# Kernel optimization log

Hardware: AMD Instinct MI355X
Metric: run time of the kernel (lower is better)

Reference implementation:

```python
import jax, jax.numpy as jnp
import numpy as np

N_SRC, N_DST = 1000, 1000
N = N_SRC + N_DST          # 2000 == feat_in of SW MLP (hard-coded in original)
D = 128                    # metapath2vec embedding dim
H = 256                    # SW hidden width
B = 100000                 # skip-gram (center, context) pairs
K = 5                      # negatives per pair
EP = 200000                # positive-graph edges
EN = 200000                # negative-graph edges


def setup_inputs() -> dict:
    key = jax.random.key(0)
    ks = jax.random.split(key, 12)
    node_embed = jax.random.normal(ks[0], (N, D), jnp.float32) * 0.1
    context_embed = jax.random.normal(ks[1], (N, D), jnp.float32) * 0.1
    # symmetric bipartite adjacency: etype plus its reverse asetype, homogenized
    A = (jax.random.uniform(ks[2], (N_SRC, N_DST)) < 0.02).astype(jnp.float32)
    adj = jnp.block([[jnp.zeros((N_SRC, N_SRC), jnp.float32), A],
                     [A.T, jnp.zeros((N_DST, N_DST), jnp.float32)]])
    W1 = jax.random.normal(ks[3], (N, H), jnp.float32) / np.sqrt(N).astype(np.float32)
    b1 = jnp.zeros((H,), jnp.float32)
    W2 = jax.random.normal(ks[4], (H, D), jnp.float32) / np.sqrt(H).astype(np.float32)
    b2 = jnp.zeros((D,), jnp.float32)
    pos_u = jax.random.randint(ks[5], (B,), 0, N)
    pos_v = jax.random.randint(ks[6], (B,), 0, N)
    neg_v = jax.random.randint(ks[7], (B, K), 0, N)
    pos_src = jax.random.randint(ks[8], (EP,), 0, N_SRC)
    pos_dst = jax.random.randint(ks[9], (EP,), 0, N_DST)
    neg_src = jax.random.randint(ks[10], (EN,), 0, N_SRC)
    neg_dst = jax.random.randint(ks[11], (EN,), 0, N_DST)
    return dict(node_embed=node_embed, context_embed=context_embed, adj=adj,
                W1=W1, b1=b1, W2=W2, b2=b2,
                pos_u=pos_u, pos_v=pos_v, neg_v=neg_v,
                pos_src=pos_src, pos_dst=pos_dst,
                neg_src=neg_src, neg_dst=neg_dst)


def _skipgram_loss(node_embed, context_embed, pos_u, pos_v, neg_v):
    # DGL MetaPath2Vec negative-sampling skip-gram loss
    emb_u = node_embed[pos_u]            # [B, D] gather
    emb_v = context_embed[pos_v]         # [B, D] gather
    pos = jnp.clip(jnp.sum(emb_u * emb_v, axis=-1), -10.0, 10.0)
    pos_loss = -jax.nn.log_sigmoid(pos)
    emb_neg = context_embed[neg_v]       # [B, K, D] gather
    neg = jnp.clip(jnp.einsum('bkd,bd->bk', emb_neg, emb_u), -10.0, 10.0)
    neg_loss = -jnp.sum(jax.nn.log_sigmoid(-neg), axis=-1)
    return jnp.mean(pos_loss + neg_loss)


def _sw_embedding(adj, feats, W1, b1, W2, b2):
    # adj @ adj @ adj * adj  /  outer(diag(adj@adj))  -> L2-row-normalized -> MLP
    A2 = adj @ adj                       # [N, N]
    part1 = (A2 @ adj) * adj             # 3-path counts masked onto existing edges
    d = jnp.diag(A2)                     # [N]
    part2 = d[:, None] * d[None, :]      # outer product of 2-path counts
    ok = part2 > 0
    gamma = jnp.where(ok, part1 / jnp.where(ok, part2, 1.0), 0.0)  # == nan_to_num
    norm = jnp.sqrt(jnp.sum(gamma * gamma, axis=-1, keepdims=True))
    gamma = gamma / jnp.maximum(norm, 1e-12)          # F.normalize(p=2, dim=1)
    sw_h = jnp.tanh(gamma @ W1 + b1) @ W2 + b2        # [N, 128]
    return jnp.concatenate([feats, sw_h], axis=1)     # [N, 256]


def reference(node_embed, context_embed, adj, W1, b1, W2, b2,
              pos_u, pos_v, neg_v, pos_src, pos_dst, neg_src, neg_dst):
    loss = _skipgram_loss(node_embed, context_embed, pos_u, pos_v, neg_v)
    # feats[etype[0]] ++ feats[etype[2]] == full node_embed table in global order
    h = _sw_embedding(adj, node_embed, W1, b1, W2, b2)
    h_src, h_dst = h[:N_SRC], h[N_SRC:]
    # HeteroDotPredictor: u_dot_v per edge -> [E, 1]
    pos_score = jnp.sum(h_src[pos_src] * h_dst[pos_dst], axis=-1, keepdims=True)
    neg_score = jnp.sum(h_src[neg_src] * h_dst[neg_dst], axis=-1, keepdims=True)
    return loss, pos_score, neg_score
```

## Files before the change

kernel.cpp:

```cpp
#include <hip/hip_runtime.h>
#include <hip/hip_bf16.h>

typedef __attribute__((ext_vector_type(8))) short bf16x8;
typedef __attribute__((ext_vector_type(4))) float f32x4;
typedef unsigned short u16;

#define BATCH 100000
#define EPE 200000

#define OFF_AP    ((size_t)0)
#define OFF_ATP   ((size_t)2097152)
#define OFF_SP    ((size_t)4194304)
#define OFF_T1    ((size_t)6291456)
#define OFF_G     ((size_t)6291456)
#define OFF_GT    ((size_t)10485760)
#define OFF_GNS   ((size_t)14680064)
#define OFF_GNDT  ((size_t)16777216)
#define OFF_W1AT  ((size_t)18874368)
#define OFF_W1BT  ((size_t)19398656)
#define OFF_W2T   ((size_t)19922944)
#define OFF_HID   ((size_t)19988480)
#define OFF_NEP   ((size_t)21037056)
#define OFF_CEP   ((size_t)21561344)
#define OFF_HSRC  ((size_t)22085632)
#define OFF_HDST  ((size_t)22609920)
#define OFF_T2    ((size_t)23134208)
#define OFF_DEGS  ((size_t)27328512)
#define OFF_DEGD  ((size_t)27332608)
#define OFF_PART  ((size_t)27336704)

__device__ __forceinline__ u16 f2b(float f) {
  union { float f; unsigned u; } v; v.f = f;
  unsigned r = v.u + 0x7fffu + ((v.u >> 16) & 1u);
  return (u16)(r >> 16);
}
__device__ __forceinline__ float b2f(u16 h) {
  union { unsigned u; float f; } v; v.u = ((unsigned)h) << 16;
  return v.f;
}

#define AS1C(p) ((const __attribute__((address_space(1))) void*)(p))
#define AS3(p)  ((__attribute__((address_space(3))) void*)(p))

__global__ __launch_bounds__(256) void prep(const float* __restrict__ adj,
    const float* __restrict__ W1, const float* __restrict__ W2,
    const float* __restrict__ ne, const float* __restrict__ ce,
    u16* __restrict__ Ap, u16* __restrict__ ATp,
    u16* __restrict__ W1At, u16* __restrict__ W1Bt, u16* __restrict__ w2t,
    u16* __restrict__ nep, u16* __restrict__ cep,
    u16* __restrict__ hsrcp, u16* __restrict__ hdstp,
    float* __restrict__ degd, float* __restrict__ degs) {
  __shared__ float tile[64][65];
  __shared__ float redf[256];
  int b = blockIdx.x;
  int t = threadIdx.x;
  int tx = t & 63, ty = t >> 6;
  if (b < 256) {
    int tr = b >> 4, tc = b & 15;
    #pragma unroll
    for (int p = 0; p < 16; p++) {
      int r = p * 4 + ty;
      int gr = tr * 64 + r, gc = tc * 64 + tx;
      float v = (gr < 1000 && gc < 1000) ? adj[(size_t)gr * 2000 + 1000 + gc] : 0.f;
      Ap[(size_t)gr * 1024 + gc] = f2b(v);
      tile[r][tx] = v;
    }
    __syncthreads();
    #pragma unroll
    for (int p = 0; p < 16; p++) {
      int r = p * 4 + ty;
      ATp[(size_t)(tc * 64 + r) * 1024 + tr * 64 + tx] = f2b(tile[tx][r]);
    }
  } else if (b < 384) {
    int b2 = b - 256;
    int half = b2 >> 6, rem = b2 & 63;
    int jt = rem >> 2, ht = rem & 3;
    #pragma unroll
    for (int p = 0; p < 16; p++) {
      int r = p * 4 + ty;
      int j = jt * 64 + r;
      tile[r][tx] = (j < 1000) ? W1[(size_t)(half * 1000 + j) * 256 + ht * 64 + tx] : 0.f;
    }
    __syncthreads();
    u16* outp = half ? W1Bt : W1At;
    #pragma unroll
    for (int p = 0; p < 16; p++) {
      int r = p * 4 + ty;
      outp[(size_t)(ht * 64 + r) * 1024 + jt * 64 + tx] = f2b(tile[tx][r]);
    }
  } else if (b < 392) {
    int b3 = b - 384;
    int dt = b3 >> 2, kt = b3 & 3;
    #pragma unroll
    for (int p = 0; p < 16; p++) {
      int r = p * 4 + ty;
      tile[r][tx] = W2[(size_t)(kt * 64 + r) * 128 + dt * 64 + tx];
    }
    __syncthreads();
    #pragma unroll
    for (int p = 0; p < 16; p++) {
      int r = p * 4 + ty;
      w2t[(size_t)(dt * 64 + r) * 256 + kt * 64 + tx] = f2b(tile[tx][r]);
    }
  } else if (b < 1416) {
    int idx = (b - 392) * 256 + t;
    int i = idx >> 7, d = idx & 127;
    float nv = (i < 2000) ? ne[(size_t)i * 128 + d] : 0.f;
    float cv = (i < 2000) ? ce[(size_t)i * 128 + d] : 0.f;
    u16 nb = f2b(nv);
    nep[idx] = nb;
    cep[idx] = f2b(cv);
    if (i < 1000)                   hsrcp[(size_t)i * 256 + d] = nb;
    else if (i < 1024)              hsrcp[(size_t)i * 256 + d] = 0;
    if (i >= 1000 && i < 2000)      hdstp[(size_t)(i - 1000) * 256 + d] = nb;
    else if (i >= 2000 && i < 2024) hdstp[(size_t)(i - 1000) * 256 + d] = 0;
  } else if (b < 1448) {
    int jb = b - 1416;
    int cx = t & 31, ry = t >> 5;
    int j = jb * 32 + cx;
    float s = 0.f;
    if (j < 1000)
      for (int i = ry; i < 1000; i += 8) s += adj[(size_t)i * 2000 + 1000 + j];
    redf[t] = s;
    __syncthreads();
    if (ry == 0) {
      float tot = 0.f;
      #pragma unroll
      for (int k = 0; k < 8; k++) tot += redf[k * 32 + cx];
      degd[j] = (j < 1000) ? tot : 0.f;
    }
  } else {
    int ib = b - 1448;
    int r = t >> 3, c8 = t & 7;
    int i = ib * 32 + r;
    float s = 0.f;
    if (i < 1000)
      for (int k = c8; k < 1000; k += 8) s += adj[(size_t)i * 2000 + 1000 + k];
    redf[t] = s;
    __syncthreads();
    if (c8 == 0) {
      float tot = 0.f;
      #pragma unroll
      for (int k = 0; k < 8; k++) tot += redf[r * 8 + k];
      degs[i] = (i < 1000) ? tot : 0.f;
    }
  }
}

template <int EPI, int MR, int NR>
__global__ __launch_bounds__(256) void gemm_bt(
    const u16* __restrict__ A, const u16* __restrict__ BT,
    const u16* __restrict__ A2, const u16* __restrict__ BT2,
    int K, int lda, int ldbt,
    u16* __restrict__ outb, int ldo,
    float* __restrict__ outf,
    const u16* __restrict__ apack,
    const float* __restrict__ degs, const float* __restrict__ degd,
    const float* __restrict__ bias,
    u16* __restrict__ hsrcp, u16* __restrict__ hdstp,
    float* __restrict__ outf2)
{
  constexpr int BMt = 32 * MR, BNt = 32 * NR;
  __shared__ u16 As[2][BMt * 64];
  __shared__ u16 Bs[2][BNt * 64];
  const int t = threadIdx.x;
  const int w = t >> 6, lane = t & 63;
  const int brow = blockIdx.x * BMt, bcol = blockIdx.y * BNt;
  const int wr = w >> 1, wc = w & 1;
  const int r16 = lane & 15, kg = lane >> 4;
  const u16* Au = (blockIdx.z == 0) ? A : A2;
  const u16* Bu = (blockIdx.z == 0) ? BT : BT2;

  f32x4 acc[MR][NR];
  #pragma unroll
  for (int m = 0; m < MR; m++)
    #pragma unroll
    for (int n = 0; n < NR; n++) {
      f32x4 z = {0.f, 0.f, 0.f, 0.f};
      acc[m][n] = z;
    }

  auto stage = [&](int buf, int k0) {
    #pragma unroll
    for (int it = 0; it < MR; ++it) {
      int chunk = it * 256 + t;
      const u16* ga = Au + (size_t)(brow + (chunk >> 3)) * lda + k0 + (chunk & 7) * 8;
      __builtin_amdgcn_global_load_lds(AS1C(ga), AS3(As[buf] + (size_t)chunk * 8), 16, 0, 0);
    }
    #pragma unroll
    for (int it = 0; it < NR; ++it) {
      int chunk = it * 256 + t;
      const u16* gb = Bu + (size_t)(bcol + (chunk >> 3)) * ldbt + k0 + (chunk & 7) * 8;
      __builtin_amdgcn_global_load_lds(AS1C(gb), AS3(Bs[buf] + (size_t)chunk * 8), 16, 0, 0);
    }
  };

  const int nst = K >> 6;
  stage(0, 0);
  int cur = 0;
  for (int s = 0; s < nst; ++s) {
    __syncthreads();
    if (s + 1 < nst) stage(cur ^ 1, (s + 1) << 6);
    const u16* Asc = As[cur];
    const u16* Bsc = Bs[cur];
    #pragma unroll
    for (int kk = 0; kk < 2; ++kk) {
      bf16x8 af[MR], bfr[NR];
      #pragma unroll
      for (int m = 0; m < MR; m++)
        af[m] = *(const bf16x8*)&Asc[(wr * (MR * 16) + m * 16 + r16) * 64 + kk * 32 + kg * 8];
      #pragma unroll
      for (int n = 0; n < NR; n++)
        bfr[n] = *(const bf16x8*)&Bsc[(wc * (NR * 16) + n * 16 + r16) * 64 + kk * 32 + kg * 8];
      #pragma unroll
      for (int m = 0; m < MR; m++)
        #pragma unroll
        for (int n = 0; n < NR; n++)
          acc[m][n] = __builtin_amdgcn_mfma_f32_16x16x32_bf16(af[m], bfr[n], acc[m][n], 0, 0, 0);
    }
    cur ^= 1;
  }

  if constexpr (EPI == 1) {
    __shared__ float gtile[32][33];
    #pragma unroll
    for (int j = 0; j < 4; j++) {
      int lr = wr * 16 + kg * 4 + j;
      int lc = wc * 16 + r16;
      int row = brow + lr, col = bcol + lc;
      float val = acc[0][0][j];
      float a = b2f(apack[(size_t)row * 1024 + col]);
      float p2 = degs[row] * degd[col];
      float g = (p2 > 0.f) ? (val * a) / p2 : 0.f;
      outf[(size_t)row * 1024 + col] = g;
      gtile[lr][lc] = g;
    }
    __syncthreads();
    #pragma unroll
    for (int p = 0; p < 4; p++) {
      int idx = p * 256 + t;
      int rr = idx >> 5, cc = idx & 31;
      outf2[(size_t)(bcol + rr) * 1024 + brow + cc] = gtile[cc][rr];
    }
    return;
  }

  #pragma unroll
  for (int m = 0; m < MR; m++) {
    #pragma unroll
    for (int n = 0; n < NR; n++) {
      #pragma unroll
      for (int j = 0; j < 4; j++) {
        int row = brow + wr * (MR * 16) + m * 16 + kg * 4 + j;
        int col = bcol + wc * (NR * 16) + n * 16 + r16;
        float val = acc[m][n][j];
        if constexpr (EPI == 0) {
          outb[(size_t)row * ldo + col] = f2b(val);
        } else if constexpr (EPI == 2) {
          outb[(size_t)(blockIdx.z * 1024 + row) * 256 + col] = f2b(tanhf(val + bias[col]));
        } else if constexpr (EPI == 3) {
          u16 hv = f2b(val + bias[col]);
          if (row < 1024) hsrcp[(size_t)row * 256 + 128 + col] = hv;
          else            hdstp[(size_t)(row - 1024) * 256 + 128 + col] = hv;
        } else if constexpr (EPI == 4) {
          outf[(size_t)row * ldo + col] = val;
        }
      }
    }
  }
}

__global__ __launch_bounds__(256) void normk(const float* __restrict__ G, const float* __restrict__ Gt,
                                             u16* __restrict__ Gns, u16* __restrict__ Gndt) {
  __shared__ float red[256];
  int b = blockIdx.x;
  const float* src = (b < 1024) ? (G + (size_t)b * 1024) : (Gt + (size_t)(b - 1024) * 1024);
  u16* dst = (b < 1024) ? (Gns + (size_t)b * 1024) : (Gndt + (size_t)(b - 1024) * 1024);
  float v[4];
  float s = 0.f;
  #pragma unroll
  for (int c = 0; c < 4; c++) { v[c] = src[threadIdx.x + 256 * c]; s += v[c] * v[c]; }
  red[threadIdx.x] = s;
  __syncthreads();
  for (int off = 128; off > 0; off >>= 1) {
    if (threadIdx.x < off) red[threadIdx.x] += red[threadIdx.x + off];
    __syncthreads();
  }
  float inv = 1.0f / fmaxf(sqrtf(red[0]), 1e-12f);
  #pragma unroll
  for (int c = 0; c < 4; c++) dst[threadIdx.x + 256 * c] = f2b(v[c] * inv);
}

__global__ __launch_bounds__(256) void skipgram_gather(const u16* __restrict__ T1,
    const int* __restrict__ pu, const int* __restrict__ pv, const int* __restrict__ nv,
    float* __restrict__ partial) {
  __shared__ float red[256];
  int s = blockIdx.x * 256 + threadIdx.x;
  float loss = 0.f;
  if (s < BATCH) {
    const u16* trow = T1 + (size_t)pu[s] * 2048;
    const int* nvb = nv + (size_t)s * 5;
    float ap = b2f(trow[pv[s]]);
    ap = fminf(fmaxf(ap, -10.f), 10.f); loss = log1pf(expf(-ap));
    #pragma unroll
    for (int k = 0; k < 5; k++) {
      float a = b2f(trow[nvb[k]]);
      a = fminf(fmaxf(a, -10.f), 10.f);
      loss += log1pf(expf(a));
    }
  }
  red[threadIdx.x] = loss;
  __syncthreads();
  for (int off = 128; off > 0; off >>= 1) {
    if (threadIdx.x < off) red[threadIdx.x] += red[threadIdx.x + off];
    __syncthreads();
  }
  if (threadIdx.x == 0) partial[blockIdx.x] = red[0];
}

__global__ __launch_bounds__(256) void edge_loss(const float* __restrict__ T2,
    const float* __restrict__ partial,
    const int* __restrict__ ps, const int* __restrict__ pd,
    const int* __restrict__ ns, const int* __restrict__ nd,
    float* __restrict__ out) {
  if (blockIdx.x == 1563) {
    __shared__ float red[256];
    float s = 0.f;
    for (int i = threadIdx.x; i < 391; i += 256) s += partial[i];
    red[threadIdx.x] = s;
    __syncthreads();
    for (int off = 128; off > 0; off >>= 1) {
      if (threadIdx.x < off) red[threadIdx.x] += red[threadIdx.x + off];
      __syncthreads();
    }
    if (threadIdx.x == 0) out[0] = red[0] / (float)BATCH;
    return;
  }
  int e = blockIdx.x * 256 + threadIdx.x;
  if (e >= 2 * EPE) return;
  int src, dst;
  if (e < EPE) { src = ps[e]; dst = pd[e]; }
  else         { src = ns[e - EPE]; dst = nd[e - EPE]; }
  out[1 + e] = T2[(size_t)src * 1024 + dst];
}

extern "C" void kernel_launch(void* const* d_in, const int* in_sizes, int n_in,
                              void* d_out, int out_size, void* d_ws, size_t ws_size,
                              hipStream_t stream) {
  const float* node_embed    = (const float*)d_in[0];
  const float* context_embed = (const float*)d_in[1];
  const float* adj           = (const float*)d_in[2];
  const float* W1            = (const float*)d_in[3];
  const float* b1            = (const float*)d_in[4];
  const float* W2            = (const float*)d_in[5];
  const float* b2            = (const float*)d_in[6];
  const int* pos_u   = (const int*)d_in[7];
  const int* pos_v   = (const int*)d_in[8];
  const int* neg_v   = (const int*)d_in[9];
  const int* pos_src = (const int*)d_in[10];
  const int* pos_dst = (const int*)d_in[11];
  const int* neg_src = (const int*)d_in[12];
  const int* neg_dst = (const int*)d_in[13];
  float* out = (float*)d_out;

  char* ws = (char*)d_ws;
  u16*   Ap    = (u16*)(ws + OFF_AP);
  u16*   ATp   = (u16*)(ws + OFF_ATP);
  u16*   Sp    = (u16*)(ws + OFF_SP);
  u16*   T1    = (u16*)(ws + OFF_T1);
  float* G     = (float*)(ws + OFF_G);
  float* Gt    = (float*)(ws + OFF_GT);
  u16*   Gns   = (u16*)(ws + OFF_GNS);
  u16*   Gndt  = (u16*)(ws + OFF_GNDT);
  u16*   W1At  = (u16*)(ws + OFF_W1AT);
  u16*   W1Bt  = (u16*)(ws + OFF_W1BT);
  u16*   w2t   = (u16*)(ws + OFF_W2T);
  u16*   hid   = (u16*)(ws + OFF_HID);
  u16*   nep   = (u16*)(ws + OFF_NEP);
  u16*   cep   = (u16*)(ws + OFF_CEP);
  u16*   hsrcp = (u16*)(ws + OFF_HSRC);
  u16*   hdstp = (u16*)(ws + OFF_HDST);
  float* T2    = (float*)(ws + OFF_T2);
  float* degs  = (float*)(ws + OFF_DEGS);
  float* degd  = (float*)(ws + OFF_DEGD);
  float* part  = (float*)(ws + OFF_PART);

  prep<<<1480, 256, 0, stream>>>(adj, W1, W2, node_embed, context_embed,
                                 Ap, ATp, W1At, W1Bt, w2t, nep, cep, hsrcp, hdstp, degd, degs);

  gemm_bt<0, 2, 2><<<dim3(32, 32), 256, 0, stream>>>(nep, cep, nullptr, nullptr, 128, 128, 128,
      T1, 2048, nullptr, nullptr, nullptr, nullptr, nullptr, nullptr, nullptr, nullptr);

  skipgram_gather<<<391, 256, 0, stream>>>(T1, pos_u, pos_v, neg_v, part);

  gemm_bt<0, 1, 1><<<dim3(32, 32), 256, 0, stream>>>(Ap, Ap, nullptr, nullptr, 1024, 1024, 1024,
      Sp, 1024, nullptr, nullptr, nullptr, nullptr, nullptr, nullptr, nullptr, nullptr);

  gemm_bt<1, 1, 1><<<dim3(32, 32), 256, 0, stream>>>(Sp, ATp, nullptr, nullptr, 1024, 1024, 1024,
      nullptr, 0, G, Ap, degs, degd, nullptr, nullptr, nullptr, Gt);

  normk<<<2048, 256, 0, stream>>>(G, Gt, Gns, Gndt);

  gemm_bt<2, 1, 1><<<dim3(32, 8, 2), 256, 0, stream>>>(Gns, W1Bt, Gndt, W1At, 1024, 1024, 1024,
      hid, 0, nullptr, nullptr, nullptr, nullptr, b1, nullptr, nullptr, nullptr);

  gemm_bt<3, 1, 1><<<dim3(64, 4), 256, 0, stream>>>(hid, w2t, nullptr, nullptr, 256, 256, 256,
      nullptr, 0, nullptr, nullptr, nullptr, nullptr, b2, hsrcp, hdstp, nullptr);

  gemm_bt<4, 1, 1><<<dim3(32, 32), 256, 0, stream>>>(hsrcp, hdstp, nullptr, nullptr, 256, 256, 256,
      nullptr, 1024, T2, nullptr, nullptr, nullptr, nullptr, nullptr, nullptr, nullptr);

  edge_loss<<<1564, 256, 0, stream>>>(T2, part, pos_src, pos_dst, neg_src, neg_dst, out);
}
```

Measured before the change: 111.3 us.

## Merge skip-gram and adjacency GEMMs into combined launches, exploit S symmetry, vectorise prep

Vectorises the prep kernel's adjacency, embedding and degree loads and stores with float4 and u16x4. The embedding-score GEMM and the A·Aᵀ GEMM now run in one launch, and the latter computes only lower-triangular 32x32 tiles, writing each tile and its transpose through shared memory. The skip-gram loss gather is folded into the launch that computes the masked 2-path product, which cuts launch count and lets independent work overlap. The T1 GEMM drops its 64x64 tile for 32x32 tiles, which means many more blocks and less reuse per block. The triangular index uses sqrt and correction loops.

```diff
diff --git a/kernel.cpp b/kernel.cpp
--- a/kernel.cpp
+++ b/kernel.cpp
@@ -3,6 +3,7 @@
 
 typedef __attribute__((ext_vector_type(8))) short bf16x8;
 typedef __attribute__((ext_vector_type(4))) float f32x4;
+typedef __attribute__((ext_vector_type(4))) unsigned short u16x4;
 typedef unsigned short u16;
 
 #define BATCH 100000
@@ -52,18 +53,25 @@
     float* __restrict__ degd, float* __restrict__ degs) {
   __shared__ float tile[64][65];
   __shared__ float redf[256];
+  __shared__ float4 red4[8][32];
   int b = blockIdx.x;
   int t = threadIdx.x;
   int tx = t & 63, ty = t >> 6;
   if (b < 256) {
     int tr = b >> 4, tc = b & 15;
-    #pragma unroll
-    for (int p = 0; p < 16; p++) {
-      int r = p * 4 + ty;
-      int gr = tr * 64 + r, gc = tc * 64 + tx;
-      float v = (gr < 1000 && gc < 1000) ? adj[(size_t)gr * 2000 + 1000 + gc] : 0.f;
-      Ap[(size_t)gr * 1024 + gc] = f2b(v);
-      tile[r][tx] = v;
+    int l16 = t & 15, rq = t >> 4;
+    #pragma unroll
+    for (int p = 0; p < 4; p++) {
+      int r = p * 16 + rq;
+      int gr = tr * 64 + r, gc0 = tc * 64 + l16 * 4;
+      float4 v = {0.f, 0.f, 0.f, 0.f};
+      if (gr < 1000 && gc0 < 1000) v = *(const float4*)&adj[(size_t)gr * 2000 + 1000 + gc0];
+      u16x4 pk = {f2b(v.x), f2b(v.y), f2b(v.z), f2b(v.w)};
+      *(u16x4*)&Ap[(size_t)gr * 1024 + gc0] = pk;
+      tile[r][l16 * 4 + 0] = v.x;
+      tile[r][l16 * 4 + 1] = v.y;
+      tile[r][l16 * 4 + 2] = v.z;
+      tile[r][l16 * 4 + 3] = v.w;
     }
     __syncthreads();
     #pragma unroll
@@ -102,40 +110,54 @@
       int r = p * 4 + ty;
       w2t[(size_t)(dt * 64 + r) * 256 + kt * 64 + tx] = f2b(tile[tx][r]);
     }
-  } else if (b < 1416) {
+  } else if (b < 648) {
     int idx = (b - 392) * 256 + t;
-    int i = idx >> 7, d = idx & 127;
-    float nv = (i < 2000) ? ne[(size_t)i * 128 + d] : 0.f;
-    float cv = (i < 2000) ? ce[(size_t)i * 128 + d] : 0.f;
-    u16 nb = f2b(nv);
-    nep[idx] = nb;
-    cep[idx] = f2b(cv);
-    if (i < 1000)                   hsrcp[(size_t)i * 256 + d] = nb;
-    else if (i < 1024)              hsrcp[(size_t)i * 256 + d] = 0;
-    if (i >= 1000 && i < 2000)      hdstp[(size_t)(i - 1000) * 256 + d] = nb;
-    else if (i >= 2000 && i < 2024) hdstp[(size_t)(i - 1000) * 256 + d] = 0;
-  } else if (b < 1448) {
-    int jb = b - 1416;
+    int i = idx >> 5, d4 = (idx & 31) * 4;
+    float4 nv = {0.f, 0.f, 0.f, 0.f}, cv = {0.f, 0.f, 0.f, 0.f};
+    if (i < 2000) {
+      nv = *(const float4*)&ne[(size_t)i * 128 + d4];
+      cv = *(const float4*)&ce[(size_t)i * 128 + d4];
+    }
+    u16x4 nb = {f2b(nv.x), f2b(nv.y), f2b(nv.z), f2b(nv.w)};
+    u16x4 cb = {f2b(cv.x), f2b(cv.y), f2b(cv.z), f2b(cv.w)};
+    u16x4 zz = {0, 0, 0, 0};
+    *(u16x4*)&nep[(size_t)i * 128 + d4] = nb;
+    *(u16x4*)&cep[(size_t)i * 128 + d4] = cb;
+    if (i < 1000)                   *(u16x4*)&hsrcp[(size_t)i * 256 + d4] = nb;
+    else if (i < 1024)              *(u16x4*)&hsrcp[(size_t)i * 256 + d4] = zz;
+    if (i >= 1000 && i < 2000)      *(u16x4*)&hdstp[(size_t)(i - 1000) * 256 + d4] = nb;
+    else if (i >= 2000 && i < 2024) *(u16x4*)&hdstp[(size_t)(i - 1000) * 256 + d4] = zz;
+  } else if (b < 656) {
+    int jb = b - 648;
     int cx = t & 31, ry = t >> 5;
-    int j = jb * 32 + cx;
-    float s = 0.f;
-    if (j < 1000)
-      for (int i = ry; i < 1000; i += 8) s += adj[(size_t)i * 2000 + 1000 + j];
-    redf[t] = s;
+    int j4 = jb * 128 + cx * 4;
+    float4 s = {0.f, 0.f, 0.f, 0.f};
+    if (j4 < 1000)
+      for (int i = ry; i < 1000; i += 8) {
+        float4 v = *(const float4*)&adj[(size_t)i * 2000 + 1000 + j4];
+        s.x += v.x; s.y += v.y; s.z += v.z; s.w += v.w;
+      }
+    red4[ry][cx] = s;
     __syncthreads();
     if (ry == 0) {
-      float tot = 0.f;
+      float4 tot = {0.f, 0.f, 0.f, 0.f};
       #pragma unroll
-      for (int k = 0; k < 8; k++) tot += redf[k * 32 + cx];
-      degd[j] = (j < 1000) ? tot : 0.f;
+      for (int k = 0; k < 8; k++) {
+        float4 v = red4[k][cx];
+        tot.x += v.x; tot.y += v.y; tot.z += v.z; tot.w += v.w;
+      }
+      *(float4*)&degd[j4] = tot;
     }
   } else {
-    int ib = b - 1448;
+    int ib = b - 656;
     int r = t >> 3, c8 = t & 7;
     int i = ib * 32 + r;
     float s = 0.f;
     if (i < 1000)
-      for (int k = c8; k < 1000; k += 8) s += adj[(size_t)i * 2000 + 1000 + k];
+      for (int k4 = c8 * 4; k4 < 1000; k4 += 32) {
+        float4 v = *(const float4*)&adj[(size_t)i * 2000 + 1000 + k4];
+        s += v.x + v.y + v.z + v.w;
+      }
     redf[t] = s;
     __syncthreads();
     if (c8 == 0) {
@@ -147,125 +169,177 @@
   }
 }
 
-template <int EPI, int MR, int NR>
+__device__ __forceinline__ f32x4 gemm_core32(const u16* __restrict__ A, const u16* __restrict__ BT,
+    int K, int lda, int ldbt, int brow, int bcol, u16* As, u16* Bs) {
+  const int t = threadIdx.x;
+  const int w = t >> 6, lane = t & 63;
+  const int wr = w >> 1, wc = w & 1;
+  const int r16 = lane & 15, kg = lane >> 4;
+  const int row = t >> 3, cc = t & 7;
+  f32x4 acc = {0.f, 0.f, 0.f, 0.f};
+  const int nst = K >> 6;
+  {
+    const u16* ga = A + (size_t)(brow + row) * lda + cc * 8;
+    __builtin_amdgcn_global_load_lds(AS1C(ga), AS3(As + t * 8), 16, 0, 0);
+    const u16* gb = BT + (size_t)(bcol + row) * ldbt + cc * 8;
+    __builtin_amdgcn_global_load_lds(AS1C(gb), AS3(Bs + t * 8), 16, 0, 0);
+  }
+  int cur = 0;
+  for (int s = 0; s < nst; ++s) {
+    __syncthreads();
+    if (s + 1 < nst) {
+      int k0 = (s + 1) << 6, nb = cur ^ 1;
+      const u16* ga = A + (size_t)(brow + row) * lda + k0 + cc * 8;
+      __builtin_amdgcn_global_load_lds(AS1C(ga), AS3(As + nb * 2048 + t * 8), 16, 0, 0);
+      const u16* gb = BT + (size_t)(bcol + row) * ldbt + k0 + cc * 8;
+      __builtin_amdgcn_global_load_lds(AS1C(gb), AS3(Bs + nb * 2048 + t * 8), 16, 0, 0);
+    }
+    const u16* Asc = As + cur * 2048;
+    const u16* Bsc = Bs + cur * 2048;
+    #pragma unroll
+    for (int kk = 0; kk < 2; ++kk) {
+      bf16x8 af = *(const bf16x8*)&Asc[(wr * 16 + r16) * 64 + kk * 32 + kg * 8];
+      bf16x8 bf_ = *(const bf16x8*)&Bsc[(wc * 16 + r16) * 64 + kk * 32 + kg * 8];
+      acc = __builtin_amdgcn_mfma_f32_16x16x32_bf16(af, bf_, acc, 0, 0, 0);
+    }
+    cur ^= 1;
+  }
+  return acc;
+}
+
+__global__ __launch_bounds__(256) void mega1(const u16* __restrict__ nep, const u16* __restrict__ cep,
+    const u16* __restrict__ Ap, u16* __restrict__ T1, u16* __restrict__ Sp) {
+  __shared__ u16 As[2 * 2048];
+  __shared__ u16 Bs[2 * 2048];
+  __shared__ u16 mir[32][33];
+  int b = blockIdx.x;
+  const int t = threadIdx.x;
+  const int w = t >> 6, lane = t & 63;
+  const int wr = w >> 1, wc = w & 1;
+  const int r16 = lane & 15, kg = lane >> 4;
+  if (b < 4096) {
+    int brow = (b >> 6) * 32, bcol = (b & 63) * 32;
+    f32x4 acc = gemm_core32(nep, cep, 128, 128, 128, brow, bcol, As, Bs);
+    #pragma unroll
+    for (int j = 0; j < 4; j++) {
+      int row = brow + wr * 16 + kg * 4 + j, col = bcol + wc * 16 + r16;
+      T1[(size_t)row * 2048 + col] = f2b(acc[j]);
+    }
+  } else {
+    int s = b - 4096;
+    int bi = (int)((sqrtf(8.f * s + 1.f) - 1.f) * 0.5f);
+    while (bi * (bi + 1) / 2 > s) bi--;
+    while ((bi + 1) * (bi + 2) / 2 <= s) bi++;
+    int bj = s - bi * (bi + 1) / 2;
+    int brow = bi * 32, bcol = bj * 32;
+    f32x4 acc = gemm_core32(Ap, Ap, 1024, 1024, 1024, brow, bcol, As, Bs);
+    #pragma unroll
+    for (int j = 0; j < 4; j++) {
+      int lr = wr * 16 + kg * 4 + j, lc = wc * 16 + r16;
+      u16 v = f2b(acc[j]);
+      Sp[(size_t)(brow + lr) * 1024 + bcol + lc] = v;
+      mir[lr][lc] = v;
+    }
+    __syncthreads();
+    #pragma unroll
+    for (int p = 0; p < 4; p++) {
+      int idx = p * 256 + t, rr = idx >> 5, cc2 = idx & 31;
+      Sp[(size_t)(bcol + rr) * 1024 + brow + cc2] = mir[cc2][rr];
+    }
+  }
+}
+
+__global__ __launch_bounds__(256) void mega2(const u16* __restrict__ Sp, const u16* __restrict__ ATp,
+    const u16* __restrict__ Ap, const float* __restrict__ degs, const float* __restrict__ degd,
+    float* __restrict__ G, float* __restrict__ Gt,
+    const u16* __restrict__ T1, const int* __restrict__ pu, const int* __restrict__ pv,
+    const int* __restrict__ nv, float* __restrict__ partial) {
+  __shared__ u16 As[2 * 2048];
+  __shared__ u16 Bs[2 * 2048];
+  __shared__ float gtile[32][33];
+  __shared__ float red[256];
+  int b = blockIdx.x;
+  const int t = threadIdx.x;
+  if (b >= 1024) {
+    int s = (b - 1024) * 256 + t;
+    float loss = 0.f;
+    if (s < BATCH) {
+      const u16* trow = T1 + (size_t)pu[s] * 2048;
+      const int* nvb = nv + (size_t)s * 5;
+      float ap = b2f(trow[pv[s]]);
+      ap = fminf(fmaxf(ap, -10.f), 10.f); loss = log1pf(expf(-ap));
+      #pragma unroll
+      for (int k = 0; k < 5; k++) {
+        float a = b2f(trow[nvb[k]]);
+        a = fminf(fmaxf(a, -10.f), 10.f);
+        loss += log1pf(expf(a));
+      }
+    }
+    red[t] = loss;
+    __syncthreads();
+    for (int off = 128; off > 0; off >>= 1) {
+      if (t < off) red[t] += red[t + off];
+      __syncthreads();
+    }
+    if (t == 0) partial[b - 1024] = red[0];
+    return;
+  }
+  const int w = t >> 6, lane = t & 63;
+  const int wr = w >> 1, wc = w & 1;
+  const int r16 = lane & 15, kg = lane >> 4;
+  int brow = (b >> 5) * 32, bcol = (b & 31) * 32;
+  f32x4 acc = gemm_core32(Sp, ATp, 1024, 1024, 1024, brow, bcol, As, Bs);
+  #pragma unroll
+  for (int j = 0; j < 4; j++) {
+    int lr = wr * 16 + kg * 4 + j, lc = wc * 16 + r16;
+    int row = brow + lr, col = bcol + lc;
+    float a = b2f(Ap[(size_t)row * 1024 + col]);
+    float p2 = degs[row] * degd[col];
+    float g = (p2 > 0.f) ? (acc[j] * a) / p2 : 0.f;
+    G[(size_t)row * 1024 + col] = g;
+    gtile[lr][lc] = g;
+  }
+  __syncthreads();
+  #pragma unroll
+  for (int p = 0; p < 4; p++) {
+    int idx = p * 256 + t, rr = idx >> 5, cc2 = idx & 31;
+    Gt[(size_t)(bcol + rr) * 1024 + brow + cc2] = gtile[cc2][rr];
+  }
+}
+
+template <int EPI>
 __global__ __launch_bounds__(256) void gemm_bt(
     const u16* __restrict__ A, const u16* __restrict__ BT,
     const u16* __restrict__ A2, const u16* __restrict__ BT2,
     int K, int lda, int ldbt,
-    u16* __restrict__ outb, int ldo,
-    float* __restrict__ outf,
-    const u16* __restrict__ apack,
-    const float* __restrict__ degs, const float* __restrict__ degd,
+    u16* __restrict__ outb,
+    float* __restrict__ outf, int ldo,
     const float* __restrict__ bias,
-    u16* __restrict__ hsrcp, u16* __restrict__ hdstp,
-    float* __restrict__ outf2)
+    u16* __restrict__ hsrcp, u16* __restrict__ hdstp)
 {
-  constexpr int BMt = 32 * MR, BNt = 32 * NR;
-  __shared__ u16 As[2][BMt * 64];
-  __shared__ u16 Bs[2][BNt * 64];
+  __shared__ u16 As[2 * 2048];
+  __shared__ u16 Bs[2 * 2048];
   const int t = threadIdx.x;
   const int w = t >> 6, lane = t & 63;
-  const int brow = blockIdx.x * BMt, bcol = blockIdx.y * BNt;
   const int wr = w >> 1, wc = w & 1;
   const int r16 = lane & 15, kg = lane >> 4;
+  const int brow = blockIdx.x * 32, bcol = blockIdx.y * 32;
   const u16* Au = (blockIdx.z == 0) ? A : A2;
   const u16* Bu = (blockIdx.z == 0) ? BT : BT2;
-
-  f32x4 acc[MR][NR];
+  f32x4 acc = gemm_core32(Au, Bu, K, lda, ldbt, brow, bcol, As, Bs);
   #pragma unroll
-  for (int m = 0; m < MR; m++)
-    #pragma unroll
-    for (int n = 0; n < NR; n++) {
-      f32x4 z = {0.f, 0.f, 0.f, 0.f};
-      acc[m][n] = z;
-    }
-
-  auto stage = [&](int buf, int k0) {
-    #pragma unroll
-    for (int it = 0; it < MR; ++it) {
-      int chunk = it * 256 + t;
-      const u16* ga = Au + (size_t)(brow + (chunk >> 3)) * lda + k0 + (chunk & 7) * 8;
-      __builtin_amdgcn_global_load_lds(AS1C(ga), AS3(As[buf] + (size_t)chunk * 8), 16, 0, 0);
-    }
-    #pragma unroll
-    for (int it = 0; it < NR; ++it) {
-      int chunk = it * 256 + t;
-      const u16* gb = Bu + (size_t)(bcol + (chunk >> 3)) * ldbt + k0 + (chunk & 7) * 8;
-      __builtin_amdgcn_global_load_lds(AS1C(gb), AS3(Bs[buf] + (size_t)chunk * 8), 16, 0, 0);
-    }
-  };
-
-  const int nst = K >> 6;
-  stage(0, 0);
-  int cur = 0;
-  for (int s = 0; s < nst; ++s) {
-    __syncthreads();
-    if (s + 1 < nst) stage(cur ^ 1, (s + 1) << 6);
-    const u16* Asc = As[cur];
-    const u16* Bsc = Bs[cur];
-    #pragma unroll
-    for (int kk = 0; kk < 2; ++kk) {
-      bf16x8 af[MR], bfr[NR];
-      #pragma unroll
-      for (int m = 0; m < MR; m++)
-        af[m] = *(const bf16x8*)&Asc[(wr * (MR * 16) + m * 16 + r16) * 64 + kk * 32 + kg * 8];
-      #pragma unroll
-      for (int n = 0; n < NR; n++)
-        bfr[n] = *(const bf16x8*)&Bsc[(wc * (NR * 16) + n * 16 + r16) * 64 + kk * 32 + kg * 8];
-      #pragma unroll
-      for (int m = 0; m < MR; m++)
-        #pragma unroll
-        for (int n = 0; n < NR; n++)
-          acc[m][n] = __builtin_amdgcn_mfma_f32_16x16x32_bf16(af[m], bfr[n], acc[m][n], 0, 0, 0);
-    }
-    cur ^= 1;
-  }
-
-  if constexpr (EPI == 1) {
-    __shared__ float gtile[32][33];
-    #pragma unroll
-    for (int j = 0; j < 4; j++) {
-      int lr = wr * 16 + kg * 4 + j;
-      int lc = wc * 16 + r16;
-      int row = brow + lr, col = bcol + lc;
-      float val = acc[0][0][j];
-      float a = b2f(apack[(size_t)row * 1024 + col]);
-      float p2 = degs[row] * degd[col];
-      float g = (p2 > 0.f) ? (val * a) / p2 : 0.f;
-      outf[(size_t)row * 1024 + col] = g;
-      gtile[lr][lc] = g;
-    }
-    __syncthreads();
-    #pragma unroll
-    for (int p = 0; p < 4; p++) {
-      int idx = p * 256 + t;
-      int rr = idx >> 5, cc = idx & 31;
-      outf2[(size_t)(bcol + rr) * 1024 + brow + cc] = gtile[cc][rr];
-    }
-    return;
-  }
-
-  #pragma unroll
-  for (int m = 0; m < MR; m++) {
-    #pragma unroll
-    for (int n = 0; n < NR; n++) {
-      #pragma unroll
-      for (int j = 0; j < 4; j++) {
-        int row = brow + wr * (MR * 16) + m * 16 + kg * 4 + j;
-        int col = bcol + wc * (NR * 16) + n * 16 + r16;
-        float val = acc[m][n][j];
-        if constexpr (EPI == 0) {
-          outb[(size_t)row * ldo + col] = f2b(val);
-        } else if constexpr (EPI == 2) {
-          outb[(size_t)(blockIdx.z * 1024 + row) * 256 + col] = f2b(tanhf(val + bias[col]));
-        } else if constexpr (EPI == 3) {
-          u16 hv = f2b(val + bias[col]);
-          if (row < 1024) hsrcp[(size_t)row * 256 + 128 + col] = hv;
-          else            hdstp[(size_t)(row - 1024) * 256 + 128 + col] = hv;
-        } else if constexpr (EPI == 4) {
-          outf[(size_t)row * ldo + col] = val;
-        }
-      }
+  for (int j = 0; j < 4; j++) {
+    int row = brow + wr * 16 + kg * 4 + j;
+    int col = bcol + wc * 16 + r16;
+    float val = acc[j];
+    if constexpr (EPI == 2) {
+      outb[(size_t)(blockIdx.z * 1024 + row) * 256 + col] = f2b(tanhf(val + bias[col]));
+    } else if constexpr (EPI == 3) {
+      u16 hv = f2b(val + bias[col]);
+      if (row < 1024) hsrcp[(size_t)row * 256 + 128 + col] = hv;
+      else            hdstp[(size_t)(row - 1024) * 256 + 128 + col] = hv;
+    } else {
+      outf[(size_t)row * ldo + col] = val;
     }
   }
 }
@@ -289,33 +363,6 @@
   float inv = 1.0f / fmaxf(sqrtf(red[0]), 1e-12f);
   #pragma unroll
   for (int c = 0; c < 4; c++) dst[threadIdx.x + 256 * c] = f2b(v[c] * inv);
-}
-
-__global__ __launch_bounds__(256) void skipgram_gather(const u16* __restrict__ T1,
-    const int* __restrict__ pu, const int* __restrict__ pv, const int* __restrict__ nv,
-    float* __restrict__ partial) {
-  __shared__ float red[256];
-  int s = blockIdx.x * 256 + threadIdx.x;
-  float loss = 0.f;
-  if (s < BATCH) {
-    const u16* trow = T1 + (size_t)pu[s] * 2048;
-    const int* nvb = nv + (size_t)s * 5;
-    float ap = b2f(trow[pv[s]]);
-    ap = fminf(fmaxf(ap, -10.f), 10.f); loss = log1pf(expf(-ap));
-    #pragma unroll
-    for (int k = 0; k < 5; k++) {
-      float a = b2f(trow[nvb[k]]);
-      a = fminf(fmaxf(a, -10.f), 10.f);
-      loss += log1pf(expf(a));
-    }
-  }
-  red[threadIdx.x] = loss;
-  __syncthreads();
-  for (int off = 128; off > 0; off >>= 1) {
-    if (threadIdx.x < off) red[threadIdx.x] += red[threadIdx.x + off];
-    __syncthreads();
-  }
-  if (threadIdx.x == 0) partial[blockIdx.x] = red[0];
 }
 
 __global__ __launch_bounds__(256) void edge_loss(const float* __restrict__ T2,
@@ -385,30 +432,24 @@
   float* degd  = (float*)(ws + OFF_DEGD);
   float* part  = (float*)(ws + OFF_PART);
 
-  prep<<<1480, 256, 0, stream>>>(adj, W1, W2, node_embed, context_embed,
-                                 Ap, ATp, W1At, W1Bt, w2t, nep, cep, hsrcp, hdstp, degd, degs);
-
-  gemm_bt<0, 2, 2><<<dim3(32, 32), 256, 0, stream>>>(nep, cep, nullptr, nullptr, 128, 128, 128,
-      T1, 2048, nullptr, nullptr, nullptr, nullptr, nullptr, nullptr, nullptr, nullptr);
-
-  skipgram_gather<<<391, 256, 0, stream>>>(T1, pos_u, pos_v, neg_v, part);
-
-  gemm_bt<0, 1, 1><<<dim3(32, 32), 256, 0, stream>>>(Ap, Ap, nullptr, nullptr, 1024, 1024, 1024,
-      Sp, 1024, nullptr, nullptr, nullptr, nullptr, nullptr, nullptr, nullptr, nullptr);
-
-  gemm_bt<1, 1, 1><<<dim3(32, 32), 256, 0, stream>>>(Sp, ATp, nullptr, nullptr, 1024, 1024, 1024,
-      nullptr, 0, G, Ap, degs, degd, nullptr, nullptr, nullptr, Gt);
+  prep<<<688, 256, 0, stream>>>(adj, W1, W2, node_embed, context_embed,
+                                Ap, ATp, W1At, W1Bt, w2t, nep, cep, hsrcp, hdstp, degd, degs);
+
+  mega1<<<4624, 256, 0, stream>>>(nep, cep, Ap, T1, Sp);
+
+  mega2<<<1415, 256, 0, stream>>>(Sp, ATp, Ap, degs, degd, G, Gt,
+                                  T1, pos_u, pos_v, neg_v, part);
 
   normk<<<2048, 256, 0, stream>>>(G, Gt, Gns, Gndt);
 
-  gemm_bt<2, 1, 1><<<dim3(32, 8, 2), 256, 0, stream>>>(Gns, W1Bt, Gndt, W1At, 1024, 1024, 1024,
-      hid, 0, nullptr, nullptr, nullptr, nullptr, b1, nullptr, nullptr, nullptr);
-
-  gemm_bt<3, 1, 1><<<dim3(64, 4), 256, 0, stream>>>(hid, w2t, nullptr, nullptr, 256, 256, 256,
-      nullptr, 0, nullptr, nullptr, nullptr, nullptr, b2, hsrcp, hdstp, nullptr);
-
-  gemm_bt<4, 1, 1><<<dim3(32, 32), 256, 0, stream>>>(hsrcp, hdstp, nullptr, nullptr, 256, 256, 256,
-      nullptr, 1024, T2, nullptr, nullptr, nullptr, nullptr, nullptr, nullptr, nullptr);
+  gemm_bt<2><<<dim3(32, 8, 2), 256, 0, stream>>>(Gns, W1Bt, Gndt, W1At, 1024, 1024, 1024,
+      hid, nullptr, 0, b1, nullptr, nullptr);
+
+  gemm_bt<3><<<dim3(64, 4), 256, 0, stream>>>(hid, w2t, nullptr, nullptr, 256, 256, 256,
+      nullptr, nullptr, 0, b2, hsrcp, hdstp);
+
+  gemm_bt<4><<<dim3(32, 32), 256, 0, stream>>>(hsrcp, hdstp, nullptr, nullptr, 256, 256, 256,
+      nullptr, T2, 1024, nullptr, nullptr, nullptr);
 
   edge_loss<<<1564, 256, 0, stream>>>(T2, part, pos_src, pos_dst, neg_src, neg_dst, out);
 }
```

After: 111.7 us. About the same (+0.3%).
